# Kernel tuning notes

Hardware: AMD Instinct MI355X
Metric: run time of the kernel (lower is better)

Reference implementation:

```python
import jax, jax.numpy as jnp
import numpy as np

N_NODES = 100000
N_EDGES = 3200000
D_FEAT = 128
HIDDEN = 64
N_CLASSES = 10
N_GRAPHS = 64


def setup_inputs() -> dict:
    key = jax.random.key(0)
    ks = jax.random.split(key, 9)
    x = jax.random.normal(ks[0], (N_NODES, D_FEAT), dtype=jnp.float32)
    edge_index = jax.random.randint(ks[1], (2, N_EDGES), 0, N_NODES, dtype=jnp.int64)
    batch = jnp.sort(jax.random.randint(ks[2], (N_NODES,), 0, N_GRAPHS, dtype=jnp.int64))
    W1 = jax.random.normal(ks[3], (D_FEAT, HIDDEN), dtype=jnp.float32) * (1.0 / np.sqrt(D_FEAT))
    b1 = jax.random.normal(ks[4], (HIDDEN,), dtype=jnp.float32) * 0.01
    W2 = jax.random.normal(ks[5], (HIDDEN, HIDDEN), dtype=jnp.float32) * (1.0 / np.sqrt(HIDDEN))
    b2 = jax.random.normal(ks[6], (HIDDEN,), dtype=jnp.float32) * 0.01
    lin_W = jax.random.normal(ks[7], (HIDDEN, N_CLASSES), dtype=jnp.float32) * (1.0 / np.sqrt(HIDDEN))
    lin_b = jax.random.normal(ks[8], (N_CLASSES,), dtype=jnp.float32) * 0.01
    return {"x": x, "edge_index": edge_index, "batch": batch,
            "W1": W1, "b1": b1, "W2": W2, "b2": b2,
            "lin_W": lin_W, "lin_b": lin_b}


def _gcn_conv(x, W, b, src, dst, norm, n_nodes):
    # x' = D^{-1/2} (A+I) D^{-1/2} X W + b  (edges already include self-loops)
    h = x @ W                                   # [N, out]
    msg = h[src] * norm[:, None]                # gather + normalize, [E+N, out]
    agg = jax.ops.segment_sum(msg, dst, num_segments=n_nodes)  # scatter-add
    return agg + b


def reference(x, edge_index, batch, W1, b1, W2, b2, lin_W, lin_b):
    n = x.shape[0]
    # add_remaining_self_loops (random edges have no self-loops w.h.p.; PyG would
    # dedupe, but appending all self-loops matches the aggregation math used here)
    loops = jnp.arange(n, dtype=edge_index.dtype)
    src = jnp.concatenate([edge_index[0], loops])
    dst = jnpp_concat = jnp.concatenate([edge_index[1], loops])
    # symmetric GCN normalization from in-degree (counts over dst)
    deg = jax.ops.segment_sum(jnp.ones_like(dst, dtype=x.dtype), dst, num_segments=n)
    dinv = jnp.where(deg > 0, jax.lax.rsqrt(jnp.maximum(deg, 1e-12)), 0.0)
    norm = dinv[src] * dinv[dst]

    h = jax.nn.relu(_gcn_conv(x, W1, b1, src, dst, norm, n))
    h = jax.nn.relu(_gcn_conv(h, W2, b2, src, dst, norm, n))

    # global mean pool over graphs in the batch
    g_sum = jax.ops.segment_sum(h, batch, num_segments=N_GRAPHS)       # [G, 64]
    g_cnt = jax.ops.segment_sum(jnp.ones((n,), dtype=h.dtype), batch, num_segments=N_GRAPHS)
    pooled = g_sum / jnp.maximum(g_cnt, 1.0)[:, None]

    logits = pooled @ lin_W + lin_b                                     # [G, C]
    return jax.nn.log_softmax(logits, axis=1)
```

## Files before the change

### kernel.cpp

```cpp
#include <hip/hip_runtime.h>
#include <hip/hip_bf16.h>

#define NNODES 100000
#define NEDGES 3200000
#define NG     64
#define NBUCK  196
#define PB     256
#define SCAN_M (PB * NBUCK)
#define SCAN_NB ((SCAN_M + 1023) / 1024)

typedef __attribute__((ext_vector_type(4))) short short4v;
typedef __attribute__((ext_vector_type(8))) short short8v;
typedef __attribute__((ext_vector_type(4))) float ffrag;

__device__ __forceinline__ int ld_idx(const void* p, long long i, int is64) {
    if (is64) return (int)((const long long*)p)[i];
    return ((const int*)p)[i];
}
__device__ __forceinline__ float ld_f(const void* p, long long i, int isf32) {
    if (isf32) return ((const float*)p)[i];
    return __bfloat162float(((const __hip_bfloat16*)p)[i]);
}
__device__ __forceinline__ float bfbits(unsigned b) {
    return __uint_as_float(b << 16);
}
__device__ __forceinline__ unsigned short bf16b(float v) {
    __hip_bfloat16 h = __float2bfloat16(v);
    return *(unsigned short*)&h;
}

__global__ void detect_kernel(const void* x, const void* ei, const void* bat, int* flags) {
    __shared__ int f[3];
    int t = threadIdx.x;
    if (t < 3) f[t] = 0;
    __syncthreads();
    const unsigned short* u = (const unsigned short*)x;
    int e = (u[t] >> 7) & 0xFF;
    if (e >= 0x90) atomicOr(&f[0], 1);
    const unsigned* w = (const unsigned*)ei;
    if (w[2 * t + 1] != 0u) atomicOr(&f[1], 1);
    const unsigned* bw = (const unsigned*)bat;
    if (bw[50001 + 2 * t] != 0u) atomicOr(&f[2], 1);
    __syncthreads();
    if (t == 0) { flags[0] = f[0]; flags[1] = !f[1]; flags[2] = !f[2]; }
}

__global__ void binA_count(const void* ei, const int* __restrict__ flags,
                           int* __restrict__ bcnt, int E) {
    __shared__ int cnt[NBUCK];
    int is64 = flags[1];
    for (int i = threadIdx.x; i < NBUCK; i += 256) cnt[i] = 0;
    __syncthreads();
    const int chunk = (E + PB - 1) / PB;
    int beg = blockIdx.x * chunk, end = min(E, beg + chunk);
    for (int i = beg + threadIdx.x; i < end; i += 256) {
        int s = ld_idx(ei, i, is64);
        int d = ld_idx(ei, (long long)E + i, is64);
        if ((unsigned)s < (unsigned)NNODES && (unsigned)d < (unsigned)NNODES)
            atomicAdd(&cnt[d >> 9], 1);
    }
    __syncthreads();
    for (int i = threadIdx.x; i < NBUCK; i += 256)
        bcnt[i * PB + blockIdx.x] = cnt[i];
}

__global__ void scanP1(int* __restrict__ a, int* __restrict__ sums) {
    __shared__ int ls[1024];
    int t = threadIdx.x;
    int i = blockIdx.x * 1024 + t;
    int v = (i < SCAN_M) ? a[i] : 0;
    ls[t] = v;
    __syncthreads();
    for (int off = 1; off < 1024; off <<= 1) {
        int p = (t >= off) ? ls[t - off] : 0;
        __syncthreads();
        ls[t] += p;
        __syncthreads();
    }
    if (i < SCAN_M) a[i] = ls[t] - v;
    if (t == 1023) sums[blockIdx.x] = ls[1023];
}

__global__ void scanP2(int* __restrict__ sums) {
    __shared__ int ls[SCAN_NB];
    int t = threadIdx.x;
    if (t < SCAN_NB) ls[t] = sums[t];
    __syncthreads();
    if (t == 0) {
        int run = 0;
        for (int i = 0; i < SCAN_NB; ++i) { int c = ls[i]; ls[i] = run; run += c; }
        sums[SCAN_NB] = run;
    }
    __syncthreads();
    if (t < SCAN_NB) sums[t] = ls[t];
}

__global__ void scanP3(int* __restrict__ a, const int* __restrict__ sums) {
    int i = blockIdx.x * 1024 + threadIdx.x;
    if (i < SCAN_M) a[i] += sums[blockIdx.x];
    if (i == 0) a[SCAN_M] = sums[SCAN_NB];
}

__global__ void binA_write(const void* ei, const int* __restrict__ flags,
                           const int* __restrict__ bcnt, unsigned* __restrict__ staging, int E) {
    __shared__ int cur[NBUCK];
    int is64 = flags[1];
    for (int i = threadIdx.x; i < NBUCK; i += 256) cur[i] = bcnt[i * PB + blockIdx.x];
    __syncthreads();
    const int chunk = (E + PB - 1) / PB;
    int beg = blockIdx.x * chunk, end = min(E, beg + chunk);
    for (int i = beg + threadIdx.x; i < end; i += 256) {
        int s = ld_idx(ei, i, is64);
        int d = ld_idx(ei, (long long)E + i, is64);
        if ((unsigned)s < (unsigned)NNODES && (unsigned)d < (unsigned)NNODES) {
            int pos = atomicAdd(&cur[d >> 9], 1);
            staging[pos] = (unsigned)s | ((unsigned)(d & 511) << 17);
        }
    }
}

__global__ void binB_all(const unsigned* __restrict__ staging, const int* __restrict__ bcnt,
                         int* __restrict__ rs, float* __restrict__ dinv,
                         int* __restrict__ csr) {
    __shared__ int dcnt[512];
    __shared__ int ls[256];
    int b = blockIdx.x;
    int lo = b << 9;
    int t = threadIdx.x;
    for (int i = t; i < 512; i += 256) dcnt[i] = 0;
    __syncthreads();
    int beg = bcnt[b * PB], end = bcnt[(b + 1) * PB];
    for (int i = beg + t; i < end; i += 256)
        atomicAdd(&dcnt[staging[i] >> 17], 1);
    __syncthreads();
    int a  = dcnt[2 * t];
    int b2 = dcnt[2 * t + 1];
    int csum = a + b2;
    ls[t] = csum;
    __syncthreads();
    for (int off = 1; off < 256; off <<= 1) {
        int p = (t >= off) ? ls[t - off] : 0;
        __syncthreads();
        ls[t] += p;
        __syncthreads();
    }
    int pref = ls[t] - csum;
    int n0 = lo + 2 * t, n1 = lo + 2 * t + 1;
    if (n0 < NNODES) { rs[n0] = beg + pref;     dinv[n0] = rsqrtf((float)a + 1.0f); }
    if (n1 < NNODES) { rs[n1] = beg + pref + a; dinv[n1] = rsqrtf((float)b2 + 1.0f); }
    if (b == NBUCK - 1 && t == 0) rs[NNODES] = bcnt[SCAN_M];
    __syncthreads();
    dcnt[2 * t]     = beg + pref;
    dcnt[2 * t + 1] = beg + pref + a;
    __syncthreads();
    for (int i = beg + t; i < end; i += 256) {
        unsigned u = staging[i];
        int pos = atomicAdd(&dcnt[u >> 17], 1);
        csr[pos] = (int)(u & 0x1FFFFu);
    }
}

template <int K, int XMODE>
__global__ __launch_bounds__(256)
void gemm_mfma(const void* __restrict__ X, const void* __restrict__ W,
               const int* __restrict__ flags, const float* __restrict__ dscale,
               __hip_bfloat16* __restrict__ Out, int N) {
    const int S = K + 4;
    __shared__ unsigned short lsWt[64 * S];
    __shared__ unsigned short lsX[64 * S];
    int isf32 = flags[0];
    for (int i = threadIdx.x; i < K * 64; i += 256) {
        int k = i >> 6, c = i & 63;
        unsigned short v = isf32 ? bf16b(((const float*)W)[i])
                                 : ((const unsigned short*)W)[i];
        lsWt[c * S + k] = v;
    }

    int lane = threadIdx.x & 63;
    int wv   = threadIdx.x >> 6;
    int m    = lane & 15;
    int quad = lane >> 4;
    int ntiles = (N + 63) >> 6;

    for (int t = blockIdx.x; t < ntiles; t += gridDim.x) {
        int row0 = t << 6;
        int nrows = min(64, N - row0);
        int nchunk = (nrows * K) >> 2;
        __syncthreads();
        if (XMODE == 0 && isf32) {
            const float4* Xb = (const float4*)((const float*)X + (long long)row0 * K);
            for (int i = threadIdx.x; i < nchunk; i += 256) {
                int r = (i << 2) / K;
                int k = (i << 2) & (K - 1);
                float4 v = Xb[i];
                uint2 o;
                o.x = (unsigned)bf16b(v.x) | ((unsigned)bf16b(v.y) << 16);
                o.y = (unsigned)bf16b(v.z) | ((unsigned)bf16b(v.w) << 16);
                *(uint2*)&lsX[r * S + k] = o;
            }
        } else {
            const uint2* Xb = (const uint2*)((const unsigned short*)X + (long long)row0 * K);
            for (int i = threadIdx.x; i < nchunk; i += 256) {
                int r = (i << 2) / K;
                int k = (i << 2) & (K - 1);
                *(uint2*)&lsX[r * S + k] = Xb[i];
            }
        }
        __syncthreads();

        int rbase = wv * 16;
        ffrag acc0 = {0.f, 0.f, 0.f, 0.f};
        ffrag acc1 = {0.f, 0.f, 0.f, 0.f};
        ffrag acc2 = {0.f, 0.f, 0.f, 0.f};
        ffrag acc3 = {0.f, 0.f, 0.f, 0.f};
        int abase = (rbase + m) * S + quad * 8;
#pragma unroll
        for (int ks = 0; ks < K; ks += 32) {
            short4v al = *(const short4v*)&lsX[abase + ks];
            short4v ah = *(const short4v*)&lsX[abase + ks + 4];
            short8v a = __builtin_shufflevector(al, ah, 0, 1, 2, 3, 4, 5, 6, 7);
#pragma unroll
            for (int ct = 0; ct < 4; ++ct) {
                int boff = (ct * 16 + m) * S + quad * 8 + ks;
                short4v bl = *(const short4v*)&lsWt[boff];
                short4v bh = *(const short4v*)&lsWt[boff + 4];
                short8v b = __builtin_shufflevector(bl, bh, 0, 1, 2, 3, 4, 5, 6, 7);
                if (ct == 0) acc0 = __builtin_amdgcn_mfma_f32_16x16x32_bf16(a, b, acc0, 0, 0, 0);
                if (ct == 1) acc1 = __builtin_amdgcn_mfma_f32_16x16x32_bf16(a, b, acc1, 0, 0, 0);
                if (ct == 2) acc2 = __builtin_amdgcn_mfma_f32_16x16x32_bf16(a, b, acc2, 0, 0, 0);
                if (ct == 3) acc3 = __builtin_amdgcn_mfma_f32_16x16x32_bf16(a, b, acc3, 0, 0, 0);
            }
        }
        long long ob = (long long)row0 * 64;
#pragma unroll
        for (int r = 0; r < 4; ++r) {
            int row = rbase + quad * 4 + r;
            if (row < nrows) {
                float ds = dscale ? dscale[row0 + row] : 1.f;
                long long rb = ob + (long long)row * 64 + m;
                Out[rb]      = __float2bfloat16(acc0[r] * ds);
                Out[rb + 16] = __float2bfloat16(acc1[r] * ds);
                Out[rb + 32] = __float2bfloat16(acc2[r] * ds);
                Out[rb + 48] = __float2bfloat16(acc3[r] * ds);
            }
        }
    }
}

template <int K, int XMODE>
__global__ __launch_bounds__(256)
void gemm_tile(const void* __restrict__ X, const void* __restrict__ W,
               const int* __restrict__ flags, const float* __restrict__ dscale,
               float* __restrict__ Out, int N) {
    __shared__ float lsW[K * 64];
    __shared__ float lsX[64 * K];
    int isf32 = flags[0];
    for (int i = threadIdx.x; i < K * 64; i += 256) lsW[i] = ld_f(W, i, isf32);
    int c  = threadIdx.x & 63;
    int wv = threadIdx.x >> 6;
    int ntiles = (N + 63) >> 6;
    for (int t = blockIdx.x; t < ntiles; t += gridDim.x) {
        int row0 = t << 6;
        int nrows = min(64, N - row0);
        int total = nrows * K;
        __syncthreads();
        if (XMODE == 1 || (XMODE == 0 && isf32)) {
            const float* Xb = (const float*)X + (long long)row0 * K;
            for (int i = threadIdx.x; i < total; i += 256) lsX[i] = Xb[i];
        } else {
            const unsigned short* Xb = (const unsigned short*)X + (long long)row0 * K;
            for (int i = threadIdx.x; i < total; i += 256) lsX[i] = bfbits((unsigned)Xb[i]);
        }
        __syncthreads();
        int rbase = wv * 16;
        float acc[16];
#pragma unroll
        for (int r = 0; r < 16; ++r) acc[r] = 0.f;
#pragma unroll 1
        for (int kc = 0; kc < K; kc += 8) {
            float w0 = lsW[(kc + 0) * 64 + c], w1 = lsW[(kc + 1) * 64 + c];
            float w2 = lsW[(kc + 2) * 64 + c], w3 = lsW[(kc + 3) * 64 + c];
            float w4 = lsW[(kc + 4) * 64 + c], w5 = lsW[(kc + 5) * 64 + c];
            float w6 = lsW[(kc + 6) * 64 + c], w7 = lsW[(kc + 7) * 64 + c];
#pragma unroll
            for (int r = 0; r < 16; ++r) {
                const float4* xp = (const float4*)&lsX[(rbase + r) * K + kc];
                float4 xa = xp[0], xb = xp[1];
                acc[r] += xa.x * w0 + xa.y * w1 + xa.z * w2 + xa.w * w3
                        + xb.x * w4 + xb.y * w5 + xb.z * w6 + xb.w * w7;
            }
        }
        long long ob = (long long)row0 * 64;
#pragma unroll
        for (int r = 0; r < 16; ++r) {
            int rr = rbase + r;
            if (rr < nrows) {
                float v = acc[r];
                if (dscale) v *= dscale[row0 + rr];
                Out[ob + (long long)rr * 64 + c] = v;
            }
        }
    }
}

__global__ __launch_bounds__(256)
void gather_v(const __hip_bfloat16* __restrict__ Hs,
              const int* __restrict__ row_start,
              const int* __restrict__ csr_src,
              const float* __restrict__ dinv,
              const void* bias, const int* __restrict__ flags,
              const float* __restrict__ out_scale,
              __hip_bfloat16* __restrict__ Hout, int N) {
    int isf32 = flags[0];
    int lane = threadIdx.x & 63;
    int e = lane >> 3;
    int f = lane & 7;
    int n = blockIdx.x * 4 + (threadIdx.x >> 6);
    if (n >= N) return;
    int beg = row_start[n], end = row_start[n + 1];

    float acc[8];
#pragma unroll
    for (int j = 0; j < 8; ++j) acc[j] = 0.f;

    for (int i = beg; i < end; i += 8) {
        int idx = i + e;
        if (idx < end) {
            int s = csr_src[idx];
            const uint4* hp = (const uint4*)(Hs + ((long long)s << 6)) + f;
            uint4 u = *hp;
            acc[0] += bfbits(u.x & 0xffffu); acc[1] += bfbits(u.x >> 16);
            acc[2] += bfbits(u.y & 0xffffu); acc[3] += bfbits(u.y >> 16);
            acc[4] += bfbits(u.z & 0xffffu); acc[5] += bfbits(u.z >> 16);
            acc[6] += bfbits(u.w & 0xffffu); acc[7] += bfbits(u.w >> 16);
        }
    }
#pragma unroll
    for (int j = 0; j < 8; ++j) {
        acc[j] += __shfl_xor(acc[j], 8);
        acc[j] += __shfl_xor(acc[j], 16);
        acc[j] += __shfl_xor(acc[j], 32);
    }
    const uint4* sp = (const uint4*)(Hs + ((long long)n << 6)) + f;
    uint4 su = *sp;
    float self[8] = { bfbits(su.x & 0xffffu), bfbits(su.x >> 16),
                      bfbits(su.y & 0xffffu), bfbits(su.y >> 16),
                      bfbits(su.z & 0xffffu), bfbits(su.z >> 16),
                      bfbits(su.w & 0xffffu), bfbits(su.w >> 16) };
    float dn = dinv[n];
    float osc = out_scale ? out_scale[n] : 1.f;
    if (e == 0) {
        unsigned short h[8];
#pragma unroll
        for (int j = 0; j < 8; ++j) {
            float v = (acc[j] + self[j]) * dn + ld_f(bias, 8 * f + j, isf32);
            float r = v > 0.f ? v : 0.f;
            h[j] = bf16b(r * osc);
        }
        uint4 o;
        o.x = (unsigned)h[0] | ((unsigned)h[1] << 16);
        o.y = (unsigned)h[2] | ((unsigned)h[3] << 16);
        o.z = (unsigned)h[4] | ((unsigned)h[5] << 16);
        o.w = (unsigned)h[6] | ((unsigned)h[7] << 16);
        *((uint4*)(Hout + ((long long)n << 6)) + f) = o;
    }
}

__global__ void pool2_bf(const __hip_bfloat16* __restrict__ H, const void* batch,
                         const int* __restrict__ flags,
                         float* __restrict__ pooled, float* __restrict__ cnt, int N) {
    __shared__ float part[NG * 64];
    __shared__ float scnt[NG];
    int b64 = flags[2];
    int tid = threadIdx.x;
    for (int i = tid; i < NG * 64; i += 256) part[i] = 0.f;
    if (tid < NG) scnt[tid] = 0.f;
    __syncthreads();
    int c = tid & 63;
    int sub = tid >> 6;
    for (int n = blockIdx.x * 4 + sub; n < N; n += gridDim.x * 4) {
        int g = ld_idx(batch, n, b64);
        if ((unsigned)g >= (unsigned)NG) continue;
        atomicAdd(&part[g * 64 + c], __bfloat162float(H[(long long)n * 64 + c]));
        if (c == 0) atomicAdd(&scnt[g], 1.0f);
    }
    __syncthreads();
    for (int i = tid; i < NG * 64; i += 256) {
        float v = part[i];
        if (v != 0.f) atomicAdd(&pooled[i], v);
    }
    if (tid < NG && scnt[tid] != 0.f) atomicAdd(&cnt[tid], scnt[tid]);
}

__global__ void final_kernel(const float* __restrict__ pooled, const float* __restrict__ cnt,
                             const void* lw, const void* lb,
                             const int* __restrict__ flags, void* out) {
    int isf32 = flags[0];
    int g = threadIdx.x;
    if (g >= NG) return;
    float inv = 1.0f / fmaxf(cnt[g], 1.0f);
    float logits[10];
    for (int c = 0; c < 10; ++c) logits[c] = ld_f(lb, c, isf32);
    for (int k = 0; k < 64; ++k) {
        float m = pooled[g * 64 + k] * inv;
        for (int c = 0; c < 10; ++c)
            logits[c] += m * ld_f(lw, k * 10 + c, isf32);
    }
    float mx = logits[0];
    for (int c = 1; c < 10; ++c) mx = fmaxf(mx, logits[c]);
    float se = 0.f;
    for (int c = 0; c < 10; ++c) se += __expf(logits[c] - mx);
    float lse = mx + __logf(se);
    if (isf32) {
        float* o = (float*)out;
        for (int c = 0; c < 10; ++c) o[g * 10 + c] = logits[c] - lse;
    } else {
        __hip_bfloat16* o = (__hip_bfloat16*)out;
        for (int c = 0; c < 10; ++c) o[g * 10 + c] = __float2bfloat16(logits[c] - lse);
    }
}

__global__ void count_kernel(const void* ei, const int* __restrict__ flags,
                             int* __restrict__ deg, int E) {
    int is64 = flags[1];
    int i = blockIdx.x * blockDim.x + threadIdx.x;
    int stride = gridDim.x * blockDim.x;
    for (; i < E; i += stride) {
        int d = ld_idx(ei, (long long)E + i, is64);
        if ((unsigned)d < (unsigned)NNODES) atomicAdd(&deg[d], 1);
    }
}

__global__ void dinv_kernel(const int* __restrict__ deg, float* __restrict__ dinv, int N) {
    int i = blockIdx.x * blockDim.x + threadIdx.x;
    if (i < N) dinv[i] = rsqrtf((float)deg[i] + 1.0f);
}

__global__ void scatter_kernel(const float* __restrict__ H, const void* ei,
                               const int* __restrict__ flags,
                               const float* __restrict__ dinv,
                               float* __restrict__ agg, int E) {
    int is64 = flags[1];
    int lane = threadIdx.x & 63;
    int e = blockIdx.x * 4 + (threadIdx.x >> 6);
    if (e >= E) return;
    int s = ld_idx(ei, e, is64);
    int d = ld_idx(ei, (long long)E + e, is64);
    if ((unsigned)s >= (unsigned)NNODES || (unsigned)d >= (unsigned)NNODES) return;
    float nrm = dinv[s] * dinv[d];
    float v = H[(long long)s * 64 + lane] * nrm;
    atomicAdd(&agg[(long long)d * 64 + lane], v);
}

__global__ void relu_bias_kernel(float* __restrict__ H, const float* __restrict__ agg,
                                 const float* __restrict__ dinv, const void* b,
                                 const int* __restrict__ flags, int N) {
    int isf32 = flags[0];
    long long idx = (long long)blockIdx.x * blockDim.x + threadIdx.x;
    if (idx >= (long long)N * 64) return;
    int n = (int)(idx >> 6);
    int c = (int)(idx & 63);
    float dv = dinv[n];
    float v = agg[idx] + H[idx] * dv * dv + ld_f(b, c, isf32);
    H[idx] = v > 0.f ? v : 0.f;
}

__global__ void pool_fb_kernel(const float* __restrict__ agg, const float* __restrict__ Hg,
                               const float* __restrict__ dinv, const void* b,
                               const void* batch, const int* __restrict__ flags,
                               float* __restrict__ pooled, float* __restrict__ cnt, int N) {
    __shared__ float part[NG * 64];
    __shared__ float scnt[NG];
    int isf32 = flags[0];
    int b64   = flags[2];
    int tid = threadIdx.x;
    for (int i = tid; i < NG * 64; i += blockDim.x) part[i] = 0.f;
    if (tid < NG) scnt[tid] = 0.f;
    __syncthreads();
    int c = tid & 63;
    int sub = tid >> 6;
    float bc = ld_f(b, c, isf32);
    for (int n = blockIdx.x * 4 + sub; n < N; n += gridDim.x * 4) {
        int g = ld_idx(batch, n, b64);
        if ((unsigned)g >= (unsigned)NG) continue;
        float dv = dinv[n];
        float v = agg[(long long)n * 64 + c] + Hg[(long long)n * 64 + c] * dv * dv + bc;
        v = v > 0.f ? v : 0.f;
        atomicAdd(&part[g * 64 + c], v);
        if (c == 0) atomicAdd(&scnt[g], 1.0f);
    }
    __syncthreads();
    for (int i = tid; i < NG * 64; i += blockDim.x) {
        float v = part[i];
        if (v != 0.f) atomicAdd(&pooled[i], v);
    }
    if (tid < NG && scnt[tid] != 0.f) atomicAdd(&cnt[tid], scnt[tid]);
}

__global__ void zero_out_kernel(unsigned short* out, int n16) {
    int i = blockIdx.x * blockDim.x + threadIdx.x;
    if (i < n16) out[i] = 0;
}

extern "C" void kernel_launch(void* const* d_in, const int* in_sizes, int n_in,
                              void* d_out, int out_size, void* d_ws, size_t ws_size,
                              hipStream_t stream) {
    const void* x   = d_in[0];
    const void* ei  = d_in[1];
    const void* bat = d_in[2];
    const void* W1  = d_in[3];
    const void* b1  = d_in[4];
    const void* W2  = d_in[5];
    const void* b2  = d_in[6];
    const void* lw  = d_in[7];
    const void* lb  = d_in[8];

    const int N = NNODES, E = NEDGES;
    int* ws = (int*)d_ws;
    const int NT = (N + 63) / 64;

    const long long o_flags = 0;
    const long long o_deg   = 16;
    const long long o_dinv  = 16 + (long long)N;
    const long long o_rs    = 16 + 2LL * N;
    const long long o_bcnt  = 300032;
    const long long o_pool  = 350272;
    const long long o_cnt   = o_pool + NG * 64;
    const long long o_csr   = 354432;
    const long long o_bufA  = o_csr + E;
    const long long o_bufB  = o_bufA + (long long)N * 64;
    const size_t need_csr = (size_t)(o_bufB + (long long)N * 64) * 4;

    const size_t need_fb = (size_t)(204800 + 2LL * N * 64) * 4;

    if (ws_size >= need_csr) {
        int*      flags   = ws + o_flags;
        int*      bsums   = ws + o_deg;
        float*    dinv    = (float*)(ws + o_dinv);
        int*      rs      = ws + o_rs;
        int*      bcnt    = ws + o_bcnt;
        float*    pooled  = (float*)(ws + o_pool);
        float*    cnt     = (float*)(ws + o_cnt);
        int*      csr     = ws + o_csr;
        unsigned* staging = (unsigned*)(ws + o_bufA);
        __hip_bfloat16* hA = (__hip_bfloat16*)(ws + o_bufA);
        __hip_bfloat16* hB = (__hip_bfloat16*)(ws + o_bufB);

        detect_kernel<<<1, 256, 0, stream>>>(x, ei, bat, flags);
        hipMemsetAsync(pooled, 0, (NG * 64 + NG) * sizeof(float), stream);

        binA_count<<<PB, 256, 0, stream>>>(ei, flags, bcnt, E);
        scanP1<<<SCAN_NB, 1024, 0, stream>>>(bcnt, bsums);
        scanP2<<<1, 64, 0, stream>>>(bsums);
        scanP3<<<SCAN_NB, 1024, 0, stream>>>(bcnt, bsums);
        binA_write<<<PB, 256, 0, stream>>>(ei, flags, bcnt, staging, E);
        binB_all<<<NBUCK, 256, 0, stream>>>(staging, bcnt, rs, dinv, csr);

        gemm_mfma<128, 0><<<NT, 256, 0, stream>>>(x, W1, flags, dinv, hA, N);
        gather_v<<<(N + 3) / 4, 256, 0, stream>>>(hA, rs, csr, dinv, b1, flags, dinv, hB, N);
        gemm_mfma<64, 2><<<NT, 256, 0, stream>>>(hB, W2, flags, nullptr, hA, N);
        gather_v<<<(N + 3) / 4, 256, 0, stream>>>(hA, rs, csr, dinv, b2, flags, nullptr, hB, N);

        pool2_bf<<<512, 256, 0, stream>>>(hB, bat, flags, pooled, cnt, N);
        final_kernel<<<1, 64, 0, stream>>>(pooled, cnt, lw, lb, flags, d_out);
    } else if (ws_size >= need_fb) {
        int*   flags  = ws;
        int*   deg    = ws + 16;
        float* dinv   = (float*)(ws + 16 + N);
        float* pooled = (float*)(ws + 16 + 2LL * N);
        float* cnt    = pooled + NG * 64;
        float* bufA   = (float*)(ws + 204800);
        float* bufB   = bufA + (long long)N * 64;

        detect_kernel<<<1, 256, 0, stream>>>(x, ei, bat, flags);
        hipMemsetAsync(deg, 0, N * sizeof(int), stream);
        hipMemsetAsync(pooled, 0, (NG * 64 + NG) * sizeof(float), stream);

        count_kernel<<<2048, 256, 0, stream>>>(ei, flags, deg, E);
        dinv_kernel<<<(N + 255) / 256, 256, 0, stream>>>(deg, dinv, N);

        gemm_tile<128, 0><<<NT, 256, 0, stream>>>(x, W1, flags, nullptr, bufA, N);
        hipMemsetAsync(bufB, 0, (size_t)N * 64 * sizeof(float), stream);
        scatter_kernel<<<(E + 3) / 4, 256, 0, stream>>>(bufA, ei, flags, dinv, bufB, E);
        relu_bias_kernel<<<((long long)N * 64 + 255) / 256, 256, 0, stream>>>(bufA, bufB, dinv, b1, flags, N);

        gemm_tile<64, 1><<<NT, 256, 0, stream>>>(bufA, W2, flags, nullptr, bufB, N);
        hipMemsetAsync(bufA, 0, (size_t)N * 64 * sizeof(float), stream);
        scatter_kernel<<<(E + 3) / 4, 256, 0, stream>>>(bufB, ei, flags, dinv, bufA, E);

        pool_fb_kernel<<<512, 256, 0, stream>>>(bufA, bufB, dinv, b2, bat, flags, pooled, cnt, N);
        final_kernel<<<1, 64, 0, stream>>>(pooled, cnt, lw, lb, flags, d_out);
    } else {
        zero_out_kernel<<<(out_size * 2 + 255) / 256, 256, 0, stream>>>(
            (unsigned short*)d_out, out_size);
    }
}
```

Before: 498.2 us.

## Fuse mean-pool into second gather and unroll edge loads four-deep

The second GCN aggregation kernel now accumulates its ReLU outputs straight into per-graph pooled sums through shared memory and global atomics. This removes the bf16 write of the hidden layer and the separate pool kernel pass. The gather loop also issues four independent neighbor row loads per iteration instead of one, to raise memory-level parallelism. The cost is more global atomics on pooled, since each block of 4 nodes issues its own adds, plus a block-wide sync in the gather.

```diff
diff --git a/kernel.cpp b/kernel.cpp
--- a/kernel.cpp
+++ b/kernel.cpp
@@ -27,6 +27,12 @@
 __device__ __forceinline__ unsigned short bf16b(float v) {
     __hip_bfloat16 h = __float2bfloat16(v);
     return *(unsigned short*)&h;
+}
+__device__ __forceinline__ void acc8(float* acc, uint4 u) {
+    acc[0] += bfbits(u.x & 0xffffu); acc[1] += bfbits(u.x >> 16);
+    acc[2] += bfbits(u.y & 0xffffu); acc[3] += bfbits(u.y >> 16);
+    acc[4] += bfbits(u.z & 0xffffu); acc[5] += bfbits(u.z >> 16);
+    acc[6] += bfbits(u.w & 0xffffu); acc[7] += bfbits(u.w >> 16);
 }
 
 __global__ void detect_kernel(const void* x, const void* ei, const void* bat, int* flags) {
@@ -303,6 +309,7 @@
     }
 }
 
+template <int POOL>
 __global__ __launch_bounds__(256)
 void gather_v(const __hip_bfloat16* __restrict__ Hs,
               const int* __restrict__ row_start,
@@ -310,30 +317,41 @@
               const float* __restrict__ dinv,
               const void* bias, const int* __restrict__ flags,
               const float* __restrict__ out_scale,
-              __hip_bfloat16* __restrict__ Hout, int N) {
+              __hip_bfloat16* __restrict__ Hout,
+              const void* batch, float* __restrict__ pooled,
+              float* __restrict__ cnt, int N) {
     int isf32 = flags[0];
     int lane = threadIdx.x & 63;
     int e = lane >> 3;
     int f = lane & 7;
-    int n = blockIdx.x * 4 + (threadIdx.x >> 6);
-    if (n >= N) return;
-    int beg = row_start[n], end = row_start[n + 1];
+    int sub = threadIdx.x >> 6;
+    int n = blockIdx.x * 4 + sub;
+    bool valid = n < N;
+    if (POOL == 0 && !valid) return;
+
+    int beg = 0, end = 0;
+    if (valid) { beg = row_start[n]; end = row_start[n + 1]; }
 
     float acc[8];
 #pragma unroll
     for (int j = 0; j < 8; ++j) acc[j] = 0.f;
 
-    for (int i = beg; i < end; i += 8) {
-        int idx = i + e;
-        if (idx < end) {
-            int s = csr_src[idx];
-            const uint4* hp = (const uint4*)(Hs + ((long long)s << 6)) + f;
-            uint4 u = *hp;
-            acc[0] += bfbits(u.x & 0xffffu); acc[1] += bfbits(u.x >> 16);
-            acc[2] += bfbits(u.y & 0xffffu); acc[3] += bfbits(u.y >> 16);
-            acc[4] += bfbits(u.z & 0xffffu); acc[5] += bfbits(u.z >> 16);
-            acc[6] += bfbits(u.w & 0xffffu); acc[7] += bfbits(u.w >> 16);
-        }
+    for (int i = beg; i < end; i += 32) {
+        int i0 = i + e;
+        int s0 = (i0      < end) ? csr_src[i0]      : -1;
+        int s1 = (i0 + 8  < end) ? csr_src[i0 + 8]  : -1;
+        int s2 = (i0 + 16 < end) ? csr_src[i0 + 16] : -1;
+        int s3 = (i0 + 24 < end) ? csr_src[i0 + 24] : -1;
+        uint4 u0 = make_uint4(0u, 0u, 0u, 0u);
+        uint4 u1 = u0, u2 = u0, u3 = u0;
+        if (s0 >= 0) u0 = *((const uint4*)(Hs + ((long long)s0 << 6)) + f);
+        if (s1 >= 0) u1 = *((const uint4*)(Hs + ((long long)s1 << 6)) + f);
+        if (s2 >= 0) u2 = *((const uint4*)(Hs + ((long long)s2 << 6)) + f);
+        if (s3 >= 0) u3 = *((const uint4*)(Hs + ((long long)s3 << 6)) + f);
+        acc8(acc, u0);
+        acc8(acc, u1);
+        acc8(acc, u2);
+        acc8(acc, u3);
     }
 #pragma unroll
     for (int j = 0; j < 8; ++j) {
@@ -341,55 +359,75 @@
         acc[j] += __shfl_xor(acc[j], 16);
         acc[j] += __shfl_xor(acc[j], 32);
     }
-    const uint4* sp = (const uint4*)(Hs + ((long long)n << 6)) + f;
-    uint4 su = *sp;
-    float self[8] = { bfbits(su.x & 0xffffu), bfbits(su.x >> 16),
-                      bfbits(su.y & 0xffffu), bfbits(su.y >> 16),
-                      bfbits(su.z & 0xffffu), bfbits(su.z >> 16),
-                      bfbits(su.w & 0xffffu), bfbits(su.w >> 16) };
-    float dn = dinv[n];
-    float osc = out_scale ? out_scale[n] : 1.f;
-    if (e == 0) {
-        unsigned short h[8];
-#pragma unroll
-        for (int j = 0; j < 8; ++j) {
-            float v = (acc[j] + self[j]) * dn + ld_f(bias, 8 * f + j, isf32);
-            float r = v > 0.f ? v : 0.f;
-            h[j] = bf16b(r * osc);
-        }
-        uint4 o;
-        o.x = (unsigned)h[0] | ((unsigned)h[1] << 16);
-        o.y = (unsigned)h[2] | ((unsigned)h[3] << 16);
-        o.z = (unsigned)h[4] | ((unsigned)h[5] << 16);
-        o.w = (unsigned)h[6] | ((unsigned)h[7] << 16);
-        *((uint4*)(Hout + ((long long)n << 6)) + f) = o;
-    }
-}
-
-__global__ void pool2_bf(const __hip_bfloat16* __restrict__ H, const void* batch,
-                         const int* __restrict__ flags,
-                         float* __restrict__ pooled, float* __restrict__ cnt, int N) {
-    __shared__ float part[NG * 64];
-    __shared__ float scnt[NG];
-    int b64 = flags[2];
-    int tid = threadIdx.x;
-    for (int i = tid; i < NG * 64; i += 256) part[i] = 0.f;
-    if (tid < NG) scnt[tid] = 0.f;
-    __syncthreads();
-    int c = tid & 63;
-    int sub = tid >> 6;
-    for (int n = blockIdx.x * 4 + sub; n < N; n += gridDim.x * 4) {
-        int g = ld_idx(batch, n, b64);
-        if ((unsigned)g >= (unsigned)NG) continue;
-        atomicAdd(&part[g * 64 + c], __bfloat162float(H[(long long)n * 64 + c]));
-        if (c == 0) atomicAdd(&scnt[g], 1.0f);
-    }
-    __syncthreads();
-    for (int i = tid; i < NG * 64; i += 256) {
-        float v = part[i];
-        if (v != 0.f) atomicAdd(&pooled[i], v);
-    }
-    if (tid < NG && scnt[tid] != 0.f) atomicAdd(&cnt[tid], scnt[tid]);
+    float self[8];
+#pragma unroll
+    for (int j = 0; j < 8; ++j) self[j] = 0.f;
+    if (valid) {
+        const uint4* sp = (const uint4*)(Hs + ((long long)n << 6)) + f;
+        uint4 su = *sp;
+        self[0] = bfbits(su.x & 0xffffu); self[1] = bfbits(su.x >> 16);
+        self[2] = bfbits(su.y & 0xffffu); self[3] = bfbits(su.y >> 16);
+        self[4] = bfbits(su.z & 0xffffu); self[5] = bfbits(su.z >> 16);
+        self[6] = bfbits(su.w & 0xffffu); self[7] = bfbits(su.w >> 16);
+    }
+    float dn = valid ? dinv[n] : 0.f;
+
+    if constexpr (POOL == 0) {
+        float osc = out_scale ? out_scale[n] : 1.f;
+        if (e == 0) {
+            unsigned short h[8];
+#pragma unroll
+            for (int j = 0; j < 8; ++j) {
+                float v = (acc[j] + self[j]) * dn + ld_f(bias, 8 * f + j, isf32);
+                float r = v > 0.f ? v : 0.f;
+                h[j] = bf16b(r * osc);
+            }
+            uint4 o;
+            o.x = (unsigned)h[0] | ((unsigned)h[1] << 16);
+            o.y = (unsigned)h[2] | ((unsigned)h[3] << 16);
+            o.z = (unsigned)h[4] | ((unsigned)h[5] << 16);
+            o.w = (unsigned)h[6] | ((unsigned)h[7] << 16);
+            *((uint4*)(Hout + ((long long)n << 6)) + f) = o;
+        }
+    } else {
+        __shared__ float pbuf[4][64];
+        __shared__ int pg[4];
+        if (valid && e == 0) {
+#pragma unroll
+            for (int j = 0; j < 8; ++j) {
+                float v = (acc[j] + self[j]) * dn + ld_f(bias, 8 * f + j, isf32);
+                pbuf[sub][8 * f + j] = v > 0.f ? v : 0.f;
+            }
+        }
+        if (lane == 0) {
+            int g = -1;
+            if (valid) {
+                g = ld_idx(batch, n, flags[2]);
+                if ((unsigned)g >= (unsigned)NG) g = -1;
+            }
+            pg[sub] = g;
+        }
+        __syncthreads();
+        int c = threadIdx.x;
+        if (c < 64) {
+            float run = 0.f;
+            int gcur = pg[0];
+#pragma unroll
+            for (int r = 0; r < 4; ++r) {
+                int g = pg[r];
+                if (g != gcur) {
+                    if (gcur >= 0 && run != 0.f) atomicAdd(&pooled[gcur * 64 + c], run);
+                    run = 0.f;
+                    gcur = g;
+                }
+                if (g >= 0) run += pbuf[r][c];
+            }
+            if (gcur >= 0 && run != 0.f) atomicAdd(&pooled[gcur * 64 + c], run);
+        } else if (c < 68) {
+            int g = pg[c - 64];
+            if (g >= 0) atomicAdd(&cnt[g], 1.0f);
+        }
+    }
 }
 
 __global__ void final_kernel(const float* __restrict__ pooled, const float* __restrict__ cnt,
@@ -557,11 +595,12 @@
         binB_all<<<NBUCK, 256, 0, stream>>>(staging, bcnt, rs, dinv, csr);
 
         gemm_mfma<128, 0><<<NT, 256, 0, stream>>>(x, W1, flags, dinv, hA, N);
-        gather_v<<<(N + 3) / 4, 256, 0, stream>>>(hA, rs, csr, dinv, b1, flags, dinv, hB, N);
+        gather_v<0><<<(N + 3) / 4, 256, 0, stream>>>(hA, rs, csr, dinv, b1, flags, dinv, hB,
+                                                     nullptr, nullptr, nullptr, N);
         gemm_mfma<64, 2><<<NT, 256, 0, stream>>>(hB, W2, flags, nullptr, hA, N);
-        gather_v<<<(N + 3) / 4, 256, 0, stream>>>(hA, rs, csr, dinv, b2, flags, nullptr, hB, N);
-
-        pool2_bf<<<512, 256, 0, stream>>>(hB, bat, flags, pooled, cnt, N);
+        gather_v<1><<<(N + 3) / 4, 256, 0, stream>>>(hA, rs, csr, dinv, b2, flags, nullptr,
+                                                     nullptr, bat, pooled, cnt, N);
+
         final_kernel<<<1, 64, 0, stream>>>(pooled, cnt, lw, lb, flags, d_out);
     } else if (ws_size >= need_fb) {
         int*   flags  = ws;
```

Result: slower. 1.270 ms (+155.0%).
